# Kernel optimization log

Hardware: AMD Instinct MI355X
Metric: run time of the kernel (lower is better)

## Reference

```python
import jax, jax.numpy as jnp
import numpy as np

# R2D2-style NghSampler2 config
NGH, SUBQ, SUBD, POS_D, NEG_D, BORDER, SUBD_NEG = 7, 8, 1, 3, 5, 16, 8

def _make_offsets():
    rad = (NGH // SUBD) * NGH
    pos, neg = [], []
    for j in range(-rad, rad + 1, SUBD):
        for i in range(-rad, rad + 1, SUBD):
            d2 = i * i + j * j
            if d2 <= POS_D ** 2:
                pos.append((i, j))
            elif NEG_D ** 2 <= d2 <= NGH ** 2:
                neg.append((i, j))
    # rows: [x(i), y(j)], matching torch .view(-1,2).t()
    return np.array(pos, np.int32).T, np.array(neg, np.int32).T

POS_OFF, NEG_OFF = _make_offsets()  # [2,29], [2,80]

def _grid(B, H, W, step):
    xs = np.arange(BORDER, W - BORDER, step)
    ys = np.arange(BORDER, H - BORDER, step)
    H1, W1 = len(ys), len(xs)
    b1 = np.repeat(np.arange(B), H1 * W1)
    y1 = np.tile(np.repeat(ys, W1), B)
    x1 = np.tile(np.tile(xs, H1), B)
    return b1, y1, x1, (B, H1, W1)

def setup_inputs() -> dict:
    key = jax.random.key(0)
    k1, k2, k3, k4, k5 = jax.random.split(key, 5)
    B, C, H, W = 4, 128, 256, 256
    feat1 = jax.random.normal(k1, (B, C, H, W), jnp.float32)
    feat2 = jax.random.normal(k2, (B, C, H, W), jnp.float32)
    conf1 = jax.random.uniform(k3, (B, 1, H, W), jnp.float32)
    conf2 = jax.random.uniform(k4, (B, 1, H, W), jnp.float32)
    aflow = jax.random.uniform(k5, (B, 2, H, W), jnp.float32) * (W - 1)
    return {"feat1": feat1, "feat2": feat2, "conf1": conf1, "conf2": conf2, "aflow": aflow}

def reference(feat1, feat2, conf1, conf2, aflow):
    B, C, H, W = feat1.shape
    b1n, y1n, x1n, shape = _grid(B, H, W, SUBQ)
    b1, y1, x1 = jnp.asarray(b1n), jnp.asarray(y1n), jnp.asarray(x1n)
    pos_off, neg_off = jnp.asarray(POS_OFF), jnp.asarray(NEG_OFF)

    f1 = feat1[b1, :, y1, x1]                      # [Q,C] query descriptors
    qconf = conf1[b1, 0, y1, x1].reshape(shape)    # [B,H1,W1]
    xy2 = (aflow[b1, :, y1, x1] + 0.5).astype(jnp.int32).T  # [2,Q] (x,y)
    mask = ((xy2[0] >= 0) & (xy2[1] >= 0) & (xy2[0] < W) & (xy2[1] < H)).reshape(shape)

    def clamp(xy):
        return jnp.stack([jnp.clip(xy[0], 0, W - 1), jnp.clip(xy[1], 0, H - 1)])

    # positives: gather feat2 at GT-correspondence + pos offsets, dot with f1
    xy2p = clamp(xy2[:, None, :] + pos_off[:, :, None])      # [2,P,Q]
    f2p = feat2[b1, :, xy2p[1], xy2p[0]]                     # [P,Q,C]
    ps_all = jnp.einsum('qc,pqc->qp', f1, f2p)               # [Q,P]
    pscores = ps_all.max(axis=1, keepdims=True)              # [Q,1]
    pos = jnp.argmax(ps_all, axis=1)                         # [Q]
    sel = clamp(xy2 + pos_off[:, pos])                       # [2,Q]
    qconf = (qconf + conf2[b1, 0, sel[1], sel[0]].reshape(shape)) / 2

    # negatives: ring of offsets around GT correspondence
    xy2n = clamp(xy2[:, None, :] + neg_off[:, :, None])      # [2,N,Q]
    f2n = feat2[b1, :, xy2n[1], xy2n[0]]                     # [N,Q,C]
    nscores = jnp.einsum('qc,nqc->qn', f1, f2n)              # [Q,N]

    # distractors on a regular grid in image 2
    b3n, y3n, x3n, _ = _grid(B, H, W, SUBD_NEG)
    b3, y3, x3 = jnp.asarray(b3n), jnp.asarray(y3n), jnp.asarray(x3n)
    distractors = feat2[b3, :, y3, x3]                       # [Q2,C]
    dscores = f1 @ distractors.T                             # [Q,Q2]
    dis2 = (x3[None, :] - xy2[0][:, None]) ** 2 \
         + (y3[None, :] - xy2[1][:, None]) ** 2 \
         + (b3[None, :] != b1[:, None]).astype(jnp.int32) * NEG_D ** 2
    dscores = jnp.where(dis2 < NEG_D ** 2, 0.0, dscores)

    scores = jnp.concatenate([pscores, nscores, dscores], axis=1)
    npos = pscores.shape[1]
    gt = jnp.concatenate([
        jnp.ones((scores.shape[0], npos), jnp.uint8),
        jnp.zeros((scores.shape[0], scores.shape[1] - npos), jnp.uint8)], axis=1)
    return scores, gt, mask, qconf
```

## Files before the change

### kernel.cpp

```cpp
#include <hip/hip_runtime.h>

#define CCH   128
#define HH    256
#define WW    256
#define BB    4
#define H1    28
#define W1    28
#define QTOT  3136
#define NPOS  29
#define NNEG  80
#define NDIS  3136
#define SCOLS 3217

typedef short s8v __attribute__((ext_vector_type(8)));
typedef float f4v __attribute__((ext_vector_type(4)));

__device__ __forceinline__ unsigned short f2bf(float f) {
  unsigned int u = __float_as_uint(f);
  u += 0x7fffu + ((u >> 16) & 1u);
  return (unsigned short)(u >> 16);
}
__device__ __forceinline__ float bflo(unsigned int v) { return __uint_as_float(v << 16); }
__device__ __forceinline__ float bfhi(unsigned int v) { return __uint_as_float(v & 0xffff0000u); }

__constant__ int POS_I[NPOS] = {
  0, -2,-1,0,1,2, -2,-1,0,1,2, -3,-2,-1,0,1,2,3, -2,-1,0,1,2, -2,-1,0,1,2, 0};
__constant__ int POS_J[NPOS] = {
  -3, -2,-2,-2,-2,-2, -1,-1,-1,-1,-1, 0,0,0,0,0,0,0, 1,1,1,1,1, 2,2,2,2,2, 3};
__constant__ int NEG_I[NNEG] = {
  0, -3,-2,-1,0,1,2,3, -4,-3,-2,-1,0,1,2,3,4, -5,-4,-3,3,4,5, -6,-5,-4,4,5,6,
  -6,-5,5,6, -6,-5,5,6, -7,-6,-5,5,6,7, -6,-5,5,6, -6,-5,5,6, -6,-5,-4,4,5,6,
  -5,-4,-3,3,4,5, -4,-3,-2,-1,0,1,2,3,4, -3,-2,-1,0,1,2,3, 0};
__constant__ int NEG_J[NNEG] = {
  -7, -6,-6,-6,-6,-6,-6,-6, -5,-5,-5,-5,-5,-5,-5,-5,-5, -4,-4,-4,-4,-4,-4,
  -3,-3,-3,-3,-3,-3, -2,-2,-2,-2, -1,-1,-1,-1, 0,0,0,0,0,0, 1,1,1,1, 2,2,2,2,
  3,3,3,3,3,3, 4,4,4,4,4,4, 5,5,5,5,5,5,5,5,5, 6,6,6,6,6,6,6, 7};

__global__ void transpose_kernel(const float* __restrict__ feat2,
                                 unsigned short* __restrict__ feat2T,
                                 unsigned short* __restrict__ F2bf) {
  __shared__ unsigned short tile[CCH][33];
  int x0 = blockIdx.x * 32;
  int y  = blockIdx.y;
  int b  = blockIdx.z;
  int tid = threadIdx.x;
  const float* src = feat2 + ((size_t)b * CCH * HH + y) * WW;
  #pragma unroll
  for (int it = 0; it < 16; ++it) {
    int idx = it * 256 + tid;
    int c = idx >> 5, xi = idx & 31;
    tile[c][xi] = f2bf(src[(size_t)c * HH * WW + x0 + xi]);
  }
  __syncthreads();
  int xi = tid >> 3, cg = (tid & 7) * 16;
  __align__(16) unsigned short tmp[16];
  #pragma unroll
  for (int k = 0; k < 16; ++k) tmp[k] = tile[cg + k][xi];
  unsigned short* dst = feat2T + ((size_t)((b * HH + y) * WW) + x0 + xi) * CCH + cg;
  *(uint4*)dst       = *(const uint4*)tmp;
  *(uint4*)(dst + 8) = *(const uint4*)(tmp + 8);

  if ((y & 7) == 0 && y >= 16 && y <= 232) {
    int xs = x0 + (tid >> 6) * 8;
    if (xs >= 16 && xs <= 232) {
      int cp = tid & 63;
      int xi2 = xs - x0;
      unsigned int lo = tile[2 * cp][xi2], hi = tile[2 * cp + 1][xi2];
      int q = b * H1 * W1 + ((y - 16) >> 3) * W1 + ((xs - 16) >> 3);
      ((unsigned int*)(F2bf + (size_t)q * CCH))[cp] = lo | (hi << 16);
    }
  }
}

__global__ void posneg_kernel(const float* __restrict__ feat1,
                              const unsigned short* __restrict__ feat2T,
                              const float* __restrict__ conf1,
                              const float* __restrict__ conf2,
                              const float* __restrict__ aflow,
                              unsigned short* __restrict__ F1bf,
                              int* __restrict__ X2, int* __restrict__ Y2,
                              float* __restrict__ mask_out,
                              float* __restrict__ scores, float* __restrict__ gt,
                              float* __restrict__ qconf_out) {
  __shared__ float f1s[CCH];
  __shared__ float posv[NPOS];
  __shared__ float negv[NNEG];
  __shared__ float bestv;
  __shared__ int sxy[2];
  int q = blockIdx.x, t = threadIdx.x;
  int b = q / (H1 * W1), r = q % (H1 * W1);
  int y = 16 + 8 * (r / W1);
  int x = 16 + 8 * (r % W1);

  if (t < CCH) {
    float v = feat1[((size_t)(b * CCH + t) * HH + y) * WW + x];
    f1s[t] = v;
    F1bf[(size_t)q * CCH + t] = f2bf(v);
  }
  if (t == 128) {
    float ax = aflow[((size_t)(b * 2 + 0) * HH + y) * WW + x];
    float ay = aflow[((size_t)(b * 2 + 1) * HH + y) * WW + x];
    int x2 = (int)(ax + 0.5f);
    int y2 = (int)(ay + 0.5f);
    X2[q] = x2; Y2[q] = y2; sxy[0] = x2; sxy[1] = y2;
    mask_out[q] = (x2 >= 0 && y2 >= 0 && x2 < WW && y2 < HH) ? 1.0f : 0.0f;
  }
  __syncthreads();
  int x2 = sxy[0], y2 = sxy[1];

  if (t < 2 * (NPOS + NNEG)) {
    int off = t >> 1, half = t & 1;
    int di = (off < NPOS) ? POS_I[off] : NEG_I[off - NPOS];
    int dj = (off < NPOS) ? POS_J[off] : NEG_J[off - NPOS];
    int xk = min(max(x2 + di, 0), WW - 1);
    int yk = min(max(y2 + dj, 0), HH - 1);
    const uint4* p4 = (const uint4*)(feat2T +
        ((size_t)((b * HH + yk) * WW) + xk) * CCH + half * 64);
    float acc = 0.f;
    #pragma unroll
    for (int i = 0; i < 8; ++i) {
      uint4 v = p4[i];
      float4 fa = *(const float4*)&f1s[half * 64 + i * 8];
      float4 fb = *(const float4*)&f1s[half * 64 + i * 8 + 4];
      acc += fa.x * bflo(v.x) + fa.y * bfhi(v.x)
           + fa.z * bflo(v.y) + fa.w * bfhi(v.y)
           + fb.x * bflo(v.z) + fb.y * bfhi(v.z)
           + fb.z * bflo(v.w) + fb.w * bfhi(v.w);
    }
    acc += __shfl_xor(acc, 1);
    if (half == 0) {
      if (off < NPOS) posv[off] = acc;
      else            negv[off - NPOS] = acc;
    }
  }
  if (t < 1 + NNEG)
    gt[(size_t)q * SCOLS + t] = (t == 0) ? 1.0f : 0.0f;
  __syncthreads();

  if (t == 0) {
    float best = posv[0]; int bi = 0;
    for (int k = 1; k < NPOS; ++k)
      if (posv[k] > best) { best = posv[k]; bi = k; }
    bestv = best;
    int sx = min(max(x2 + POS_I[bi], 0), WW - 1);
    int sy = min(max(y2 + POS_J[bi], 0), HH - 1);
    float c1 = conf1[((size_t)b * HH + y) * WW + x];
    float c2 = conf2[((size_t)b * HH + sy) * WW + sx];
    qconf_out[q] = 0.5f * (c1 + c2);
  }
  __syncthreads();

  if (t < 1 + NNEG)
    scores[(size_t)q * SCOLS + t] = (t == 0) ? bestv : negv[t - 1];
}

__global__ void dscore_kernel(const unsigned short* __restrict__ F1bf,
                              const unsigned short* __restrict__ F2bf,
                              const int* __restrict__ X2, const int* __restrict__ Y2,
                              float* __restrict__ scores, float* __restrict__ gt) {
  __shared__ float tile[64][66];
  __shared__ int sx2[64], sy2[64];
  int w = threadIdx.x >> 6, lane = threadIdx.x & 63;
  int qb = blockIdx.y * 64;
  int db = blockIdx.x * 64;
  int m  = lane & 15;
  int ko = (lane >> 4) * 8;

  if (threadIdx.x < 64) {
    sx2[threadIdx.x] = X2[qb + threadIdx.x];
    sy2[threadIdx.x] = Y2[qb + threadIdx.x];
  }

  f4v acc[4];
  #pragma unroll
  for (int dt = 0; dt < 4; ++dt) acc[dt] = (f4v){0.f, 0.f, 0.f, 0.f};

  #pragma unroll
  for (int kk = 0; kk < 4; ++kk) {
    s8v a = *(const s8v*)(F1bf + (size_t)(qb + w * 16 + m) * CCH + kk * 32 + ko);
    #pragma unroll
    for (int dt = 0; dt < 4; ++dt) {
      s8v bfr = *(const s8v*)(F2bf + (size_t)(db + dt * 16 + m) * CCH + kk * 32 + ko);
      acc[dt] = __builtin_amdgcn_mfma_f32_16x16x32_bf16(a, bfr, acc[dt], 0, 0, 0);
    }
  }

  int rbase = (lane >> 4) * 4, col = lane & 15;
  #pragma unroll
  for (int dt = 0; dt < 4; ++dt)
    #pragma unroll
    for (int r = 0; r < 4; ++r)
      tile[w * 16 + rbase + r][dt * 16 + col] = acc[dt][r];
  __syncthreads();

  int d = db + lane;
  int dbat = d / (H1 * W1), dr = d % (H1 * W1);
  int dy = 16 + 8 * (dr / W1), dx = 16 + 8 * (dr % W1);

  #pragma unroll
  for (int i = 0; i < 16; ++i) {
    int row = w * 16 + i;
    int q = qb + row;
    int qbat = q / (H1 * W1);
    int ddx = dx - sx2[row], ddy = dy - sy2[row];
    int dis2 = ddx * ddx + ddy * ddy + (dbat != qbat ? 25 : 0);
    float v = tile[row][lane];
    if (dis2 < 25) v = 0.f;
    size_t o = (size_t)q * SCOLS + 1 + NNEG + d;
    scores[o] = v;
    gt[o] = 0.f;
  }
}

extern "C" void kernel_launch(void* const* d_in, const int* in_sizes, int n_in,
                              void* d_out, int out_size, void* d_ws, size_t ws_size,
                              hipStream_t stream) {
  const float* feat1 = (const float*)d_in[0];
  const float* feat2 = (const float*)d_in[1];
  const float* conf1 = (const float*)d_in[2];
  const float* conf2 = (const float*)d_in[3];
  const float* aflow = (const float*)d_in[4];

  float* out       = (float*)d_out;
  float* scores    = out;
  float* gt        = out + (size_t)QTOT * SCOLS;
  float* mask_out  = out + 2 * (size_t)QTOT * SCOLS;
  float* qconf_out = mask_out + QTOT;

  unsigned short* feat2T = (unsigned short*)d_ws;
  unsigned short* F1bf   = feat2T + (size_t)BB * HH * WW * CCH;
  unsigned short* F2bf   = F1bf + (size_t)QTOT * CCH;
  int* X2 = (int*)(F2bf + (size_t)QTOT * CCH);
  int* Y2 = X2 + QTOT;

  dim3 gT(WW / 32, HH, BB);
  transpose_kernel<<<gT, 256, 0, stream>>>(feat2, feat2T, F2bf);
  posneg_kernel<<<QTOT, 256, 0, stream>>>(feat1, feat2T, conf1, conf2, aflow,
                                          F1bf, X2, Y2, mask_out, scores, gt, qconf_out);
  dim3 gD(NDIS / 64, QTOT / 64);
  dscore_kernel<<<gD, 256, 0, stream>>>(F1bf, F2bf, X2, Y2, scores, gt);
}
```

Before: 339.7 us.

## Merge posneg and dscore kernels, move query feature gather into transpose

The query-feature bf16 conversion and the flow/mask computation move into the transpose kernel. The posneg and distractor-score kernels become one launch that branches on block index, so both kinds of work can run concurrently and one launch boundary is removed. The transpose loads are widened to float4, and the large score/gt stores become nontemporal. In exchange, positive/negative dots now use bf16-rounded query features instead of fp32, and the merged kernel uses a shared-memory union sized for the larger branch.

```diff
diff --git a/kernel.cpp b/kernel.cpp
--- a/kernel.cpp
+++ b/kernel.cpp
@@ -10,6 +10,8 @@
 #define NPOS  29
 #define NNEG  80
 #define NDIS  3136
+#define DT64  (NDIS / 64)
+#define QT64  (QTOT / 64)
 #define SCOLS 3217
 
 typedef short s8v __attribute__((ext_vector_type(8)));
@@ -37,8 +39,13 @@
   3,3,3,3,3,3, 4,4,4,4,4,4, 5,5,5,5,5,5,5,5,5, 6,6,6,6,6,6,6, 7};
 
 __global__ void transpose_kernel(const float* __restrict__ feat2,
+                                 const float* __restrict__ feat1,
+                                 const float* __restrict__ aflow,
                                  unsigned short* __restrict__ feat2T,
-                                 unsigned short* __restrict__ F2bf) {
+                                 unsigned short* __restrict__ F1bf,
+                                 unsigned short* __restrict__ F2bf,
+                                 int* __restrict__ X2, int* __restrict__ Y2,
+                                 float* __restrict__ mask_out) {
   __shared__ unsigned short tile[CCH][33];
   int x0 = blockIdx.x * 32;
   int y  = blockIdx.y;
@@ -46,10 +53,15 @@
   int tid = threadIdx.x;
   const float* src = feat2 + ((size_t)b * CCH * HH + y) * WW;
   #pragma unroll
-  for (int it = 0; it < 16; ++it) {
+  for (int it = 0; it < 4; ++it) {
     int idx = it * 256 + tid;
-    int c = idx >> 5, xi = idx & 31;
-    tile[c][xi] = f2bf(src[(size_t)c * HH * WW + x0 + xi]);
+    int c = idx >> 3, xq = idx & 7;
+    float4 v = ((const float4*)(src + (size_t)c * HH * WW + x0))[xq];
+    int xb = xq * 4;
+    tile[c][xb + 0] = f2bf(v.x);
+    tile[c][xb + 1] = f2bf(v.y);
+    tile[c][xb + 2] = f2bf(v.z);
+    tile[c][xb + 3] = f2bf(v.w);
   }
   __syncthreads();
   int xi = tid >> 3, cg = (tid & 7) * 16;
@@ -64,151 +76,151 @@
     int xs = x0 + (tid >> 6) * 8;
     if (xs >= 16 && xs <= 232) {
       int cp = tid & 63;
+      int q = b * H1 * W1 + ((y - 16) >> 3) * W1 + ((xs - 16) >> 3);
       int xi2 = xs - x0;
       unsigned int lo = tile[2 * cp][xi2], hi = tile[2 * cp + 1][xi2];
-      int q = b * H1 * W1 + ((y - 16) >> 3) * W1 + ((xs - 16) >> 3);
       ((unsigned int*)(F2bf + (size_t)q * CCH))[cp] = lo | (hi << 16);
+      const float* f1p = feat1 + ((size_t)(b * CCH + 2 * cp) * HH + y) * WW + xs;
+      unsigned int l1 = f2bf(f1p[0]);
+      unsigned int h1 = f2bf(f1p[(size_t)HH * WW]);
+      ((unsigned int*)(F1bf + (size_t)q * CCH))[cp] = l1 | (h1 << 16);
+      if (cp == 0) {
+        float ax = aflow[((size_t)(b * 2 + 0) * HH + y) * WW + xs];
+        float ay = aflow[((size_t)(b * 2 + 1) * HH + y) * WW + xs];
+        int x2 = (int)(ax + 0.5f);
+        int y2 = (int)(ay + 0.5f);
+        X2[q] = x2; Y2[q] = y2;
+        mask_out[q] = (x2 >= 0 && y2 >= 0 && x2 < WW && y2 < HH) ? 1.0f : 0.0f;
+      }
     }
   }
 }
 
-__global__ void posneg_kernel(const float* __restrict__ feat1,
-                              const unsigned short* __restrict__ feat2T,
-                              const float* __restrict__ conf1,
-                              const float* __restrict__ conf2,
-                              const float* __restrict__ aflow,
-                              unsigned short* __restrict__ F1bf,
-                              int* __restrict__ X2, int* __restrict__ Y2,
-                              float* __restrict__ mask_out,
-                              float* __restrict__ scores, float* __restrict__ gt,
-                              float* __restrict__ qconf_out) {
-  __shared__ float f1s[CCH];
-  __shared__ float posv[NPOS];
-  __shared__ float negv[NNEG];
-  __shared__ float bestv;
-  __shared__ int sxy[2];
-  int q = blockIdx.x, t = threadIdx.x;
-  int b = q / (H1 * W1), r = q % (H1 * W1);
-  int y = 16 + 8 * (r / W1);
-  int x = 16 + 8 * (r % W1);
-
-  if (t < CCH) {
-    float v = feat1[((size_t)(b * CCH + t) * HH + y) * WW + x];
-    f1s[t] = v;
-    F1bf[(size_t)q * CCH + t] = f2bf(v);
-  }
-  if (t == 128) {
-    float ax = aflow[((size_t)(b * 2 + 0) * HH + y) * WW + x];
-    float ay = aflow[((size_t)(b * 2 + 1) * HH + y) * WW + x];
-    int x2 = (int)(ax + 0.5f);
-    int y2 = (int)(ay + 0.5f);
-    X2[q] = x2; Y2[q] = y2; sxy[0] = x2; sxy[1] = y2;
-    mask_out[q] = (x2 >= 0 && y2 >= 0 && x2 < WW && y2 < HH) ? 1.0f : 0.0f;
-  }
-  __syncthreads();
-  int x2 = sxy[0], y2 = sxy[1];
-
-  if (t < 2 * (NPOS + NNEG)) {
-    int off = t >> 1, half = t & 1;
-    int di = (off < NPOS) ? POS_I[off] : NEG_I[off - NPOS];
-    int dj = (off < NPOS) ? POS_J[off] : NEG_J[off - NPOS];
-    int xk = min(max(x2 + di, 0), WW - 1);
-    int yk = min(max(y2 + dj, 0), HH - 1);
-    const uint4* p4 = (const uint4*)(feat2T +
-        ((size_t)((b * HH + yk) * WW) + xk) * CCH + half * 64);
-    float acc = 0.f;
-    #pragma unroll
-    for (int i = 0; i < 8; ++i) {
-      uint4 v = p4[i];
-      float4 fa = *(const float4*)&f1s[half * 64 + i * 8];
-      float4 fb = *(const float4*)&f1s[half * 64 + i * 8 + 4];
-      acc += fa.x * bflo(v.x) + fa.y * bfhi(v.x)
-           + fa.z * bflo(v.y) + fa.w * bfhi(v.y)
-           + fb.x * bflo(v.z) + fb.y * bfhi(v.z)
-           + fb.z * bflo(v.w) + fb.w * bfhi(v.w);
-    }
-    acc += __shfl_xor(acc, 1);
-    if (half == 0) {
-      if (off < NPOS) posv[off] = acc;
-      else            negv[off - NPOS] = acc;
-    }
-  }
-  if (t < 1 + NNEG)
-    gt[(size_t)q * SCOLS + t] = (t == 0) ? 1.0f : 0.0f;
-  __syncthreads();
-
-  if (t == 0) {
-    float best = posv[0]; int bi = 0;
-    for (int k = 1; k < NPOS; ++k)
-      if (posv[k] > best) { best = posv[k]; bi = k; }
-    bestv = best;
-    int sx = min(max(x2 + POS_I[bi], 0), WW - 1);
-    int sy = min(max(y2 + POS_J[bi], 0), HH - 1);
-    float c1 = conf1[((size_t)b * HH + y) * WW + x];
-    float c2 = conf2[((size_t)b * HH + sy) * WW + sx];
-    qconf_out[q] = 0.5f * (c1 + c2);
-  }
-  __syncthreads();
-
-  if (t < 1 + NNEG)
-    scores[(size_t)q * SCOLS + t] = (t == 0) ? bestv : negv[t - 1];
-}
-
-__global__ void dscore_kernel(const unsigned short* __restrict__ F1bf,
-                              const unsigned short* __restrict__ F2bf,
-                              const int* __restrict__ X2, const int* __restrict__ Y2,
-                              float* __restrict__ scores, float* __restrict__ gt) {
-  __shared__ float tile[64][66];
-  __shared__ int sx2[64], sy2[64];
-  int w = threadIdx.x >> 6, lane = threadIdx.x & 63;
-  int qb = blockIdx.y * 64;
-  int db = blockIdx.x * 64;
-  int m  = lane & 15;
-  int ko = (lane >> 4) * 8;
-
-  if (threadIdx.x < 64) {
-    sx2[threadIdx.x] = X2[qb + threadIdx.x];
-    sy2[threadIdx.x] = Y2[qb + threadIdx.x];
-  }
-
-  f4v acc[4];
-  #pragma unroll
-  for (int dt = 0; dt < 4; ++dt) acc[dt] = (f4v){0.f, 0.f, 0.f, 0.f};
-
-  #pragma unroll
-  for (int kk = 0; kk < 4; ++kk) {
-    s8v a = *(const s8v*)(F1bf + (size_t)(qb + w * 16 + m) * CCH + kk * 32 + ko);
-    #pragma unroll
-    for (int dt = 0; dt < 4; ++dt) {
-      s8v bfr = *(const s8v*)(F2bf + (size_t)(db + dt * 16 + m) * CCH + kk * 32 + ko);
-      acc[dt] = __builtin_amdgcn_mfma_f32_16x16x32_bf16(a, bfr, acc[dt], 0, 0, 0);
-    }
-  }
-
-  int rbase = (lane >> 4) * 4, col = lane & 15;
-  #pragma unroll
-  for (int dt = 0; dt < 4; ++dt)
-    #pragma unroll
-    for (int r = 0; r < 4; ++r)
-      tile[w * 16 + rbase + r][dt * 16 + col] = acc[dt][r];
-  __syncthreads();
-
-  int d = db + lane;
-  int dbat = d / (H1 * W1), dr = d % (H1 * W1);
-  int dy = 16 + 8 * (dr / W1), dx = 16 + 8 * (dr % W1);
-
-  #pragma unroll
-  for (int i = 0; i < 16; ++i) {
-    int row = w * 16 + i;
-    int q = qb + row;
-    int qbat = q / (H1 * W1);
-    int ddx = dx - sx2[row], ddy = dy - sy2[row];
-    int dis2 = ddx * ddx + ddy * ddy + (dbat != qbat ? 25 : 0);
-    float v = tile[row][lane];
-    if (dis2 < 25) v = 0.f;
-    size_t o = (size_t)q * SCOLS + 1 + NNEG + d;
-    scores[o] = v;
-    gt[o] = 0.f;
+__global__ void main_kernel(const unsigned short* __restrict__ feat2T,
+                            const float* __restrict__ conf1,
+                            const float* __restrict__ conf2,
+                            const unsigned short* __restrict__ F1bf,
+                            const unsigned short* __restrict__ F2bf,
+                            const int* __restrict__ X2, const int* __restrict__ Y2,
+                            float* __restrict__ scores, float* __restrict__ gt,
+                            float* __restrict__ qconf_out) {
+  __shared__ union {
+    struct { float tile[64][66]; int sx2[64]; int sy2[64]; } ds;
+    struct { __align__(16) float f1s[CCH]; float posv[NPOS]; float negv[NNEG];
+             float bestv; } pn;
+  } sm;
+
+  if (blockIdx.x < QTOT) {
+    int q = blockIdx.x, t = threadIdx.x;
+    int b = q / (H1 * W1), r = q % (H1 * W1);
+    int y = 16 + 8 * (r / W1);
+    int x = 16 + 8 * (r % W1);
+
+    if (t < 64) {
+      unsigned int u = ((const unsigned int*)(F1bf + (size_t)q * CCH))[t];
+      sm.pn.f1s[2 * t]     = bflo(u);
+      sm.pn.f1s[2 * t + 1] = bfhi(u);
+    }
+    int x2 = X2[q], y2 = Y2[q];
+    __syncthreads();
+
+    if (t < 2 * (NPOS + NNEG)) {
+      int off = t >> 1, half = t & 1;
+      int di = (off < NPOS) ? POS_I[off] : NEG_I[off - NPOS];
+      int dj = (off < NPOS) ? POS_J[off] : NEG_J[off - NPOS];
+      int xk = min(max(x2 + di, 0), WW - 1);
+      int yk = min(max(y2 + dj, 0), HH - 1);
+      const uint4* p4 = (const uint4*)(feat2T +
+          ((size_t)((b * HH + yk) * WW) + xk) * CCH + half * 64);
+      float acc = 0.f;
+      #pragma unroll
+      for (int i = 0; i < 8; ++i) {
+        uint4 v = p4[i];
+        float4 fa = *(const float4*)&sm.pn.f1s[half * 64 + i * 8];
+        float4 fb = *(const float4*)&sm.pn.f1s[half * 64 + i * 8 + 4];
+        acc += fa.x * bflo(v.x) + fa.y * bfhi(v.x)
+             + fa.z * bflo(v.y) + fa.w * bfhi(v.y)
+             + fb.x * bflo(v.z) + fb.y * bfhi(v.z)
+             + fb.z * bflo(v.w) + fb.w * bfhi(v.w);
+      }
+      acc += __shfl_xor(acc, 1);
+      if (half == 0) {
+        if (off < NPOS) sm.pn.posv[off] = acc;
+        else            sm.pn.negv[off - NPOS] = acc;
+      }
+    }
+    if (t < 1 + NNEG)
+      gt[(size_t)q * SCOLS + t] = (t == 0) ? 1.0f : 0.0f;
+    __syncthreads();
+
+    if (t == 0) {
+      float best = sm.pn.posv[0]; int bi = 0;
+      for (int k = 1; k < NPOS; ++k)
+        if (sm.pn.posv[k] > best) { best = sm.pn.posv[k]; bi = k; }
+      sm.pn.bestv = best;
+      int sx = min(max(x2 + POS_I[bi], 0), WW - 1);
+      int sy = min(max(y2 + POS_J[bi], 0), HH - 1);
+      float c1 = conf1[((size_t)b * HH + y) * WW + x];
+      float c2 = conf2[((size_t)b * HH + sy) * WW + sx];
+      qconf_out[q] = 0.5f * (c1 + c2);
+    }
+    __syncthreads();
+
+    if (t < 1 + NNEG)
+      scores[(size_t)q * SCOLS + t] = (t == 0) ? sm.pn.bestv : sm.pn.negv[t - 1];
+
+  } else {
+    int bid = blockIdx.x - QTOT;
+    int qb = (bid / DT64) * 64;
+    int db = (bid % DT64) * 64;
+    int w = threadIdx.x >> 6, lane = threadIdx.x & 63;
+    int m  = lane & 15;
+    int ko = (lane >> 4) * 8;
+
+    if (threadIdx.x < 64) {
+      sm.ds.sx2[threadIdx.x] = X2[qb + threadIdx.x];
+      sm.ds.sy2[threadIdx.x] = Y2[qb + threadIdx.x];
+    }
+
+    f4v acc[4];
+    #pragma unroll
+    for (int dt = 0; dt < 4; ++dt) acc[dt] = (f4v){0.f, 0.f, 0.f, 0.f};
+
+    #pragma unroll
+    for (int kk = 0; kk < 4; ++kk) {
+      s8v a = *(const s8v*)(F1bf + (size_t)(qb + w * 16 + m) * CCH + kk * 32 + ko);
+      #pragma unroll
+      for (int dt = 0; dt < 4; ++dt) {
+        s8v bfr = *(const s8v*)(F2bf + (size_t)(db + dt * 16 + m) * CCH + kk * 32 + ko);
+        acc[dt] = __builtin_amdgcn_mfma_f32_16x16x32_bf16(a, bfr, acc[dt], 0, 0, 0);
+      }
+    }
+
+    int rbase = (lane >> 4) * 4, col = lane & 15;
+    #pragma unroll
+    for (int dt = 0; dt < 4; ++dt)
+      #pragma unroll
+      for (int r = 0; r < 4; ++r)
+        sm.ds.tile[w * 16 + rbase + r][dt * 16 + col] = acc[dt][r];
+    __syncthreads();
+
+    int d = db + lane;
+    int dbat = d / (H1 * W1), dr = d % (H1 * W1);
+    int dy = 16 + 8 * (dr / W1), dx = 16 + 8 * (dr % W1);
+
+    #pragma unroll
+    for (int i = 0; i < 16; ++i) {
+      int row = w * 16 + i;
+      int q = qb + row;
+      int qbat = q / (H1 * W1);
+      int ddx = dx - sm.ds.sx2[row], ddy = dy - sm.ds.sy2[row];
+      int dis2 = ddx * ddx + ddy * ddy + (dbat != qbat ? 25 : 0);
+      float v = sm.ds.tile[row][lane];
+      if (dis2 < 25) v = 0.f;
+      size_t o = (size_t)q * SCOLS + 1 + NNEG + d;
+      __builtin_nontemporal_store(v,   &scores[o]);
+      __builtin_nontemporal_store(0.f, &gt[o]);
+    }
   }
 }
 
@@ -234,9 +246,9 @@
   int* Y2 = X2 + QTOT;
 
   dim3 gT(WW / 32, HH, BB);
-  transpose_kernel<<<gT, 256, 0, stream>>>(feat2, feat2T, F2bf);
-  posneg_kernel<<<QTOT, 256, 0, stream>>>(feat1, feat2T, conf1, conf2, aflow,
-                                          F1bf, X2, Y2, mask_out, scores, gt, qconf_out);
-  dim3 gD(NDIS / 64, QTOT / 64);
-  dscore_kernel<<<gD, 256, 0, stream>>>(F1bf, F2bf, X2, Y2, scores, gt);
-}
+  transpose_kernel<<<gT, 256, 0, stream>>>(feat2, feat1, aflow, feat2T,
+                                           F1bf, F2bf, X2, Y2, mask_out);
+  main_kernel<<<QTOT + DT64 * QT64, 256, 0, stream>>>(feat2T, conf1, conf2,
+                                                      F1bf, F2bf, X2, Y2,
+                                                      scores, gt, qconf_out);
+}
```

Measured after the change: 339.5 us. Within noise of the previous version (-0.0%).
